# Kernel tuning notes

Hardware: AMD Instinct MI355X
Metric: run time of the kernel (lower is better)

The kernel has to match this reference:

```python
import jax, jax.numpy as jnp
import numpy as np

N = 50000      # nodes
E = 800000     # edges (avg degree 16)
D_IN = 128
D_OUT = 128


def setup_inputs() -> dict:
    key = jax.random.key(0)
    k = jax.random.split(key, 6)
    x = jax.random.normal(k[0], (N, D_IN), dtype=jnp.float32)
    rows = jax.random.randint(k[1], (E,), 0, N, dtype=jnp.int32)   # destination nodes
    cols = jax.random.randint(k[2], (E,), 0, N, dtype=jnp.int32)   # source nodes
    vals = jax.random.uniform(k[3], (E,), dtype=jnp.float32)       # adj edge weights
    W = jax.random.normal(k[4], (D_OUT, D_IN), dtype=jnp.float32) * (1.0 / np.sqrt(D_IN))
    b = jax.random.normal(k[5], (D_OUT,), dtype=jnp.float32) * 0.01
    return {"x": x, "rows": rows, "cols": cols, "vals": vals, "W": W, "b": b}


def reference(x, rows, cols, vals, W, b):
    # Linear: h = x @ W^T + b   (torch nn.Linear convention, W: [out, in])
    h = jnp.einsum("ni,oi->no", x, W) + b            # [N, D_OUT]
    # spmm(adj, h): out[i] = sum_{(i,j) in E} vals_ij * h[j]
    msgs = h[cols] * vals[:, None]                    # [E, D_OUT]
    out = jax.ops.segment_sum(msgs, rows, num_segments=N)  # [N, D_OUT]
    return out
```

## Files before the change

kernel.cpp:

```cpp
#include <hip/hip_runtime.h>

#define D 128
#define SCAN_BLK 256
#define SCAN_THREADS 1024

typedef short  bf16x8 __attribute__((ext_vector_type(8)));
typedef float  f32x4  __attribute__((ext_vector_type(4)));

static __device__ __forceinline__ unsigned short f2bf(float f) {
    unsigned u = __float_as_uint(f);
    u += 0x7FFFu + ((u >> 16) & 1u);
    return (unsigned short)(u >> 16);
}
static __device__ __forceinline__ float bf2f_lo(unsigned u) {
    return __uint_as_float((u & 0xFFFFu) << 16);
}
static __device__ __forceinline__ float bf2f_hi(unsigned u) {
    return __uint_as_float(u & 0xFFFF0000u);
}

__global__ __launch_bounds__(256) void fused_pre(
    const int* __restrict__ rows, int* __restrict__ counts, int n_edges,
    const float* __restrict__ W, unsigned short* __restrict__ Wb, int histBlocks) {
    int bid = blockIdx.x;
    if (bid < histBlocks) {
        int i = bid * 256 + threadIdx.x;
        if (i < n_edges) atomicAdd(&counts[rows[i]], 1);
    } else {
        int i = (bid - histBlocks) * 256 + threadIdx.x;
        if (i < D * D) Wb[i] = f2bf(W[i]);
    }
}

__global__ __launch_bounds__(256) void fused_main(
    const int* __restrict__ rows, const int* __restrict__ cols,
    const float* __restrict__ vals, int* __restrict__ cursor,
    int2* __restrict__ evec, int n_edges, int permBlocks,
    const float* __restrict__ x, const unsigned short* __restrict__ Wb,
    const float* __restrict__ b, unsigned short* __restrict__ hb, int n_rows) {
    int bid = blockIdx.x;
    if (bid < permBlocks) {
        int i = bid * 256 + threadIdx.x;
        if (i >= n_edges) return;
        int r   = rows[i];
        int pos = atomicAdd(&cursor[r], 1);
        evec[pos] = make_int2(cols[i], __float_as_int(vals[i]));
        return;
    }

    const int gb   = bid - permBlocks;
    const int lane = threadIdx.x & 63;
    const int wv   = threadIdx.x >> 6;
    const int row0 = gb * 64 + wv * 16;
    if (row0 >= n_rows) return;
    const int m  = lane & 15;
    const int kg = lane >> 4;

    int arow = row0 + m;
    if (arow >= n_rows) arow = n_rows - 1;
    const float* xr = x + (size_t)arow * D + kg * 8;

    f32x4 acc[8];
#pragma unroll
    for (int n = 0; n < 8; ++n) acc[n] = (f32x4){0.f, 0.f, 0.f, 0.f};

#pragma unroll
    for (int ks = 0; ks < 4; ++ks) {
        float4 f0 = *(const float4*)(xr + ks * 32);
        float4 f1 = *(const float4*)(xr + ks * 32 + 4);
        bf16x8 a;
        a[0] = (short)f2bf(f0.x); a[1] = (short)f2bf(f0.y);
        a[2] = (short)f2bf(f0.z); a[3] = (short)f2bf(f0.w);
        a[4] = (short)f2bf(f1.x); a[5] = (short)f2bf(f1.y);
        a[6] = (short)f2bf(f1.z); a[7] = (short)f2bf(f1.w);
#pragma unroll
        for (int n = 0; n < 8; ++n) {
            bf16x8 bf = *(const bf16x8*)&Wb[(size_t)(n * 16 + m) * D + ks * 32 + kg * 8];
            acc[n] = __builtin_amdgcn_mfma_f32_16x16x32_bf16(a, bf, acc[n], 0, 0, 0);
        }
    }

#pragma unroll
    for (int n = 0; n < 8; ++n) {
        int col = n * 16 + m;
        float bc = b[col];
#pragma unroll
        for (int j = 0; j < 4; ++j) {
            int r = row0 + kg * 4 + j;
            if (r < n_rows) hb[(size_t)r * D + col] = f2bf(acc[n][j] + bc);
        }
    }
}

__global__ __launch_bounds__(SCAN_BLK) void scan_local(
    const int* __restrict__ counts, int* __restrict__ offs,
    int* __restrict__ blockSums, int n) {
    __shared__ int sh[SCAN_BLK];
    const int t = threadIdx.x;
    const int i = blockIdx.x * SCAN_BLK + t;
    int v = (i < n) ? counts[i] : 0;
    sh[t] = v;
    __syncthreads();
    for (int off = 1; off < SCAN_BLK; off <<= 1) {
        int add = (t >= off) ? sh[t - off] : 0;
        __syncthreads();
        sh[t] += add;
        __syncthreads();
    }
    if (i < n) offs[i] = sh[t] - v;
    if (t == SCAN_BLK - 1) blockSums[blockIdx.x] = sh[SCAN_BLK - 1];
}

__global__ __launch_bounds__(1024) void scan_blocks(
    int* __restrict__ blockSums, int* __restrict__ total, int nb) {
    __shared__ int sh[1024];
    const int t = threadIdx.x;
    int v = (t < nb) ? blockSums[t] : 0;
    sh[t] = v;
    __syncthreads();
    for (int off = 1; off < 1024; off <<= 1) {
        int add = (t >= off) ? sh[t - off] : 0;
        __syncthreads();
        sh[t] += add;
        __syncthreads();
    }
    if (t < nb) blockSums[t] = sh[t] - v;
    if (t == 1023) *total = sh[1023];
}

__global__ __launch_bounds__(SCAN_BLK) void scan_add(
    int* __restrict__ offs, int* __restrict__ cursor,
    const int* __restrict__ blockSums, int n) {
    const int i = blockIdx.x * SCAN_BLK + threadIdx.x;
    if (i < n) {
        int o = offs[i] + blockSums[blockIdx.x];
        offs[i]   = o;
        cursor[i] = o;
    }
}

__global__ __launch_bounds__(SCAN_THREADS) void scan_counts(
    const int* __restrict__ counts, int* __restrict__ offs,
    int* __restrict__ cursor, int n) {
    __shared__ int part[SCAN_THREADS];
    const int t = threadIdx.x;
    const int chunk = (n + SCAN_THREADS - 1) / SCAN_THREADS;
    const int s = t * chunk;
    const int e = min(s + chunk, n);
    int sum = 0;
    for (int i = s; i < e; ++i) sum += counts[i];
    part[t] = sum;
    __syncthreads();
    for (int off = 1; off < SCAN_THREADS; off <<= 1) {
        int add = (t >= off) ? part[t - off] : 0;
        __syncthreads();
        part[t] += add;
        __syncthreads();
    }
    int run = part[t] - sum;
    for (int i = s; i < e; ++i) {
        offs[i]   = run;
        cursor[i] = run;
        run += counts[i];
    }
    if (e == n) offs[n] = run;
}

__global__ __launch_bounds__(256) void aggregate(
    const int* __restrict__ offs, const int2* __restrict__ evec,
    const unsigned short* __restrict__ hb, float* __restrict__ out, int n_nodes) {
    int wid = blockIdx.x * (blockDim.x >> 6) + (threadIdx.x >> 6);
    if (wid >= n_nodes) return;
    int lane = threadIdx.x & 63;

    int s = offs[wid];
    int e = offs[wid + 1];
    float2 acc = make_float2(0.f, 0.f);

    int k = s;
    if ((k & 1) && k < e) {
        int2 e0 = evec[k];
        unsigned u0 = *(const unsigned*)&hb[(size_t)e0.x * D + lane * 2];
        float v0 = __int_as_float(e0.y);
        acc.x += v0 * bf2f_lo(u0); acc.y += v0 * bf2f_hi(u0);
        ++k;
    }
    for (; k + 3 < e; k += 4) {
        int4 p0 = *(const int4*)&evec[k];
        int4 p1 = *(const int4*)&evec[k + 2];
        unsigned u0 = *(const unsigned*)&hb[(size_t)p0.x * D + lane * 2];
        unsigned u1 = *(const unsigned*)&hb[(size_t)p0.z * D + lane * 2];
        unsigned u2 = *(const unsigned*)&hb[(size_t)p1.x * D + lane * 2];
        unsigned u3 = *(const unsigned*)&hb[(size_t)p1.z * D + lane * 2];
        float v0 = __int_as_float(p0.y);
        float v1 = __int_as_float(p0.w);
        float v2 = __int_as_float(p1.y);
        float v3 = __int_as_float(p1.w);
        acc.x += v0 * bf2f_lo(u0); acc.y += v0 * bf2f_hi(u0);
        acc.x += v1 * bf2f_lo(u1); acc.y += v1 * bf2f_hi(u1);
        acc.x += v2 * bf2f_lo(u2); acc.y += v2 * bf2f_hi(u2);
        acc.x += v3 * bf2f_lo(u3); acc.y += v3 * bf2f_hi(u3);
    }
    for (; k < e; ++k) {
        int2 e0 = evec[k];
        unsigned u0 = *(const unsigned*)&hb[(size_t)e0.x * D + lane * 2];
        float v0 = __int_as_float(e0.y);
        acc.x += v0 * bf2f_lo(u0); acc.y += v0 * bf2f_hi(u0);
    }

    *(float2*)&out[(size_t)wid * D + lane * 2] = acc;
}

__global__ __launch_bounds__(256) void scatter_add(
    const int* __restrict__ rows, const int* __restrict__ cols,
    const float* __restrict__ vals, const unsigned short* __restrict__ hb,
    float* __restrict__ out, int n_edges) {
    long long gid = (long long)blockIdx.x * blockDim.x + threadIdx.x;
    int e  = (int)(gid >> 5);
    if (e >= n_edges) return;
    int d4 = ((int)gid & 31) * 4;
    int   r = rows[e];
    int   c = cols[e];
    float v = vals[e];
    const unsigned short* hp = &hb[(size_t)c * D + d4];
    unsigned u0 = *(const unsigned*)(hp + 0);
    unsigned u1 = *(const unsigned*)(hp + 2);
    float* op = &out[(size_t)r * D + d4];
    atomicAdd(op + 0, v * bf2f_lo(u0));
    atomicAdd(op + 1, v * bf2f_hi(u0));
    atomicAdd(op + 2, v * bf2f_lo(u1));
    atomicAdd(op + 3, v * bf2f_hi(u1));
}

__global__ void convert_W(const float* __restrict__ W, unsigned short* __restrict__ Wb) {
    int i = blockIdx.x * blockDim.x + threadIdx.x;
    if (i < D * D) Wb[i] = f2bf(W[i]);
}

__global__ __launch_bounds__(256) void gemm_mfma(
    const float* __restrict__ x, const unsigned short* __restrict__ Wb,
    const float* __restrict__ b, unsigned short* __restrict__ hb, int n_rows) {
    const int lane = threadIdx.x & 63;
    const int wv   = threadIdx.x >> 6;
    const int row0 = blockIdx.x * 64 + wv * 16;
    if (row0 >= n_rows) return;
    const int m  = lane & 15;
    const int kg = lane >> 4;
    int arow = row0 + m;
    if (arow >= n_rows) arow = n_rows - 1;
    const float* xr = x + (size_t)arow * D + kg * 8;
    f32x4 acc[8];
#pragma unroll
    for (int n = 0; n < 8; ++n) acc[n] = (f32x4){0.f, 0.f, 0.f, 0.f};
#pragma unroll
    for (int ks = 0; ks < 4; ++ks) {
        float4 f0 = *(const float4*)(xr + ks * 32);
        float4 f1 = *(const float4*)(xr + ks * 32 + 4);
        bf16x8 a;
        a[0] = (short)f2bf(f0.x); a[1] = (short)f2bf(f0.y);
        a[2] = (short)f2bf(f0.z); a[3] = (short)f2bf(f0.w);
        a[4] = (short)f2bf(f1.x); a[5] = (short)f2bf(f1.y);
        a[6] = (short)f2bf(f1.z); a[7] = (short)f2bf(f1.w);
#pragma unroll
        for (int n = 0; n < 8; ++n) {
            bf16x8 bf = *(const bf16x8*)&Wb[(size_t)(n * 16 + m) * D + ks * 32 + kg * 8];
            acc[n] = __builtin_amdgcn_mfma_f32_16x16x32_bf16(a, bf, acc[n], 0, 0, 0);
        }
    }
#pragma unroll
    for (int n = 0; n < 8; ++n) {
        int col = n * 16 + m;
        float bc = b[col];
#pragma unroll
        for (int j = 0; j < 4; ++j) {
            int r = row0 + kg * 4 + j;
            if (r < n_rows) hb[(size_t)r * D + col] = f2bf(acc[n][j] + bc);
        }
    }
}

static inline size_t align16(size_t x) { return (x + 15) & ~(size_t)15; }

extern "C" void kernel_launch(void* const* d_in, const int* in_sizes, int n_in,
                              void* d_out, int out_size, void* d_ws, size_t ws_size,
                              hipStream_t stream) {
    const float* x    = (const float*)d_in[0];
    const int*   rows = (const int*)  d_in[1];
    const int*   cols = (const int*)  d_in[2];
    const float* vals = (const float*)d_in[3];
    const float* W    = (const float*)d_in[4];
    const float* b    = (const float*)d_in[5];
    float*       out  = (float*)d_out;

    const int n_nodes = in_sizes[0] / D;
    const int n_edges = in_sizes[1];
    const int nScanBlocks = (n_nodes + SCAN_BLK - 1) / SCAN_BLK;
    const int histBlocks  = (n_edges + 255) / 256;
    const int convBlocks  = (D * D + 255) / 256;
    const int gemmBlocks  = (n_nodes + 63) / 64;

    char*  base    = (char*)d_ws;
    size_t off     = 0;
    unsigned short* Wb = (unsigned short*)(base + off); off = align16(off + (size_t)D * D * 2);
    unsigned short* hb = (unsigned short*)(base + off); off = align16(off + (size_t)n_nodes * D * 2);
    int*   counts  = (int*)  (base + off); off = align16(off + (size_t)n_nodes * 4);
    int*   offs    = (int*)  (base + off); off = align16(off + ((size_t)n_nodes + 1) * 4);
    int*   cursor  = (int*)  (base + off); off = align16(off + (size_t)n_nodes * 4);
    int*   bsums   = (int*)  (base + off); off = align16(off + (size_t)1024 * 4);
    int2*  evec    = (int2*) (base + off); off = align16(off + (size_t)n_edges * 8);
    const bool csr_fits = (off <= ws_size);

    if (csr_fits) {
        hipMemsetAsync(counts, 0, (size_t)n_nodes * 4, stream);
        fused_pre<<<histBlocks + convBlocks, 256, 0, stream>>>(
            rows, counts, n_edges, W, Wb, histBlocks);
        if (nScanBlocks <= 1024) {
            scan_local<<<nScanBlocks, SCAN_BLK, 0, stream>>>(counts, offs, bsums, n_nodes);
            scan_blocks<<<1, 1024, 0, stream>>>(bsums, &offs[n_nodes], nScanBlocks);
            scan_add<<<nScanBlocks, SCAN_BLK, 0, stream>>>(offs, cursor, bsums, n_nodes);
        } else {
            scan_counts<<<1, SCAN_THREADS, 0, stream>>>(counts, offs, cursor, n_nodes);
        }
        fused_main<<<histBlocks + gemmBlocks, 256, 0, stream>>>(
            rows, cols, vals, cursor, evec, n_edges, histBlocks,
            x, Wb, b, hb, n_nodes);
        aggregate<<<(n_nodes + 3) / 4, 256, 0, stream>>>(offs, evec, hb, out, n_nodes);
    } else {
        convert_W<<<convBlocks, 256, 0, stream>>>(W, Wb);
        gemm_mfma<<<gemmBlocks, 256, 0, stream>>>(x, Wb, b, hb, n_nodes);
        hipMemsetAsync(d_out, 0, (size_t)n_nodes * D * sizeof(float), stream);
        long long scatter_threads = (long long)n_edges * 32;
        int scatter_blocks = (int)((scatter_threads + 255) / 256);
        scatter_add<<<scatter_blocks, 256, 0, stream>>>(rows, cols, vals, hb, out, n_edges);
    }
}
```

Baseline: 175.1 us.

## Interleave permutation and GEMM blocks in fused kernel; unroll aggregate by 8

```diff
diff --git a/kernel.cpp b/kernel.cpp
--- a/kernel.cpp
+++ b/kernel.cpp
@@ -35,20 +35,25 @@
 __global__ __launch_bounds__(256) void fused_main(
     const int* __restrict__ rows, const int* __restrict__ cols,
     const float* __restrict__ vals, int* __restrict__ cursor,
-    int2* __restrict__ evec, int n_edges, int permBlocks,
+    int2* __restrict__ evec, int n_edges, int permSlots,
     const float* __restrict__ x, const unsigned short* __restrict__ Wb,
     const float* __restrict__ b, unsigned short* __restrict__ hb, int n_rows) {
-    int bid = blockIdx.x;
-    if (bid < permBlocks) {
-        int i = bid * 256 + threadIdx.x;
-        if (i >= n_edges) return;
-        int r   = rows[i];
-        int pos = atomicAdd(&cursor[r], 1);
-        evec[pos] = make_int2(cols[i], __float_as_int(vals[i]));
+    const int bid = blockIdx.x;
+    const int g   = bid / 5;
+    const int r5  = bid % 5;
+
+    if (r5 >= 2) {
+        const int slot   = g * 3 + (r5 - 2);
+        const int stride = permSlots * 256;
+        for (int i = slot * 256 + threadIdx.x; i < n_edges; i += stride) {
+            int rr  = rows[i];
+            int pos = atomicAdd(&cursor[rr], 1);
+            evec[pos] = make_int2(cols[i], __float_as_int(vals[i]));
+        }
         return;
     }
 
-    const int gb   = bid - permBlocks;
+    const int gb   = g * 2 + r5;
     const int lane = threadIdx.x & 63;
     const int wv   = threadIdx.x >> 6;
     const int row0 = gb * 64 + wv * 16;
@@ -86,8 +91,8 @@
         float bc = b[col];
 #pragma unroll
         for (int j = 0; j < 4; ++j) {
-            int r = row0 + kg * 4 + j;
-            if (r < n_rows) hb[(size_t)r * D + col] = f2bf(acc[n][j] + bc);
+            int rr = row0 + kg * 4 + j;
+            if (rr < n_rows) hb[(size_t)rr * D + col] = f2bf(acc[n][j] + bc);
         }
     }
 }
@@ -185,23 +190,41 @@
         acc.x += v0 * bf2f_lo(u0); acc.y += v0 * bf2f_hi(u0);
         ++k;
     }
-    for (; k + 3 < e; k += 4) {
+    for (; k + 7 < e; k += 8) {
         int4 p0 = *(const int4*)&evec[k];
         int4 p1 = *(const int4*)&evec[k + 2];
+        int4 p2 = *(const int4*)&evec[k + 4];
+        int4 p3 = *(const int4*)&evec[k + 6];
         unsigned u0 = *(const unsigned*)&hb[(size_t)p0.x * D + lane * 2];
         unsigned u1 = *(const unsigned*)&hb[(size_t)p0.z * D + lane * 2];
         unsigned u2 = *(const unsigned*)&hb[(size_t)p1.x * D + lane * 2];
         unsigned u3 = *(const unsigned*)&hb[(size_t)p1.z * D + lane * 2];
-        float v0 = __int_as_float(p0.y);
-        float v1 = __int_as_float(p0.w);
-        float v2 = __int_as_float(p1.y);
-        float v3 = __int_as_float(p1.w);
+        unsigned u4 = *(const unsigned*)&hb[(size_t)p2.x * D + lane * 2];
+        unsigned u5 = *(const unsigned*)&hb[(size_t)p2.z * D + lane * 2];
+        unsigned u6 = *(const unsigned*)&hb[(size_t)p3.x * D + lane * 2];
+        unsigned u7 = *(const unsigned*)&hb[(size_t)p3.z * D + lane * 2];
+        float v0 = __int_as_float(p0.y), v1 = __int_as_float(p0.w);
+        float v2 = __int_as_float(p1.y), v3 = __int_as_float(p1.w);
+        float v4 = __int_as_float(p2.y), v5 = __int_as_float(p2.w);
+        float v6 = __int_as_float(p3.y), v7 = __int_as_float(p3.w);
         acc.x += v0 * bf2f_lo(u0); acc.y += v0 * bf2f_hi(u0);
         acc.x += v1 * bf2f_lo(u1); acc.y += v1 * bf2f_hi(u1);
         acc.x += v2 * bf2f_lo(u2); acc.y += v2 * bf2f_hi(u2);
         acc.x += v3 * bf2f_lo(u3); acc.y += v3 * bf2f_hi(u3);
-    }
-    for (; k < e; ++k) {
+        acc.x += v4 * bf2f_lo(u4); acc.y += v4 * bf2f_hi(u4);
+        acc.x += v5 * bf2f_lo(u5); acc.y += v5 * bf2f_hi(u5);
+        acc.x += v6 * bf2f_lo(u6); acc.y += v6 * bf2f_hi(u6);
+        acc.x += v7 * bf2f_lo(u7); acc.y += v7 * bf2f_hi(u7);
+    }
+    for (; k + 1 < e; k += 2) {
+        int4 p0 = *(const int4*)&evec[k];
+        unsigned u0 = *(const unsigned*)&hb[(size_t)p0.x * D + lane * 2];
+        unsigned u1 = *(const unsigned*)&hb[(size_t)p0.z * D + lane * 2];
+        float v0 = __int_as_float(p0.y), v1 = __int_as_float(p0.w);
+        acc.x += v0 * bf2f_lo(u0); acc.y += v0 * bf2f_hi(u0);
+        acc.x += v1 * bf2f_lo(u1); acc.y += v1 * bf2f_hi(u1);
+    }
+    if (k < e) {
         int2 e0 = evec[k];
         unsigned u0 = *(const unsigned*)&hb[(size_t)e0.x * D + lane * 2];
         float v0 = __int_as_float(e0.y);
@@ -298,6 +321,9 @@
     const int histBlocks  = (n_edges + 255) / 256;
     const int convBlocks  = (D * D + 255) / 256;
     const int gemmBlocks  = (n_nodes + 63) / 64;
+    const int nGroups     = (gemmBlocks + 1) / 2;
+    const int permSlots   = nGroups * 3;
+    const int mainBlocks  = nGroups * 5;
 
     char*  base    = (char*)d_ws;
     size_t off     = 0;
@@ -321,8 +347,8 @@
         } else {
             scan_counts<<<1, SCAN_THREADS, 0, stream>>>(counts, offs, cursor, n_nodes);
         }
-        fused_main<<<histBlocks + gemmBlocks, 256, 0, stream>>>(
-            rows, cols, vals, cursor, evec, n_edges, histBlocks,
+        fused_main<<<mainBlocks, 256, 0, stream>>>(
+            rows, cols, vals, cursor, evec, n_edges, permSlots,
             x, Wb, b, hb, n_nodes);
         aggregate<<<(n_nodes + 3) / 4, 256, 0, stream>>>(offs, evec, hb, out, n_nodes);
     } else {
```

Result: faster. 141.4 us (-19.3%).
